# Kernel tuning notes

Hardware: AMD Instinct MI355X
Metric: run time of the kernel (lower is better)

Reference implementation:

```python
import jax, jax.numpy as jnp
import numpy as np

H = 256   # hidden_size
IN = 2    # adding-problem input features
B, T = 128, 1024


def setup_inputs() -> dict:
    key = jax.random.key(0)
    ks = jax.random.split(key, 12)
    sc = 1.0 / np.sqrt(H)
    u = lambda k, shape: jax.random.uniform(k, shape, minval=-sc, maxval=sc, dtype=jnp.float32)
    return {
        "x": jax.random.normal(ks[0], (B, T, IN), dtype=jnp.float32),
        # GRU weights (torch layout: [3H, in], gate order r, z, n)
        "W_ih": u(ks[1], (3 * H, IN)),
        "W_hh": u(ks[2], (3 * H, H)),
        "b_ih": u(ks[3], (3 * H,)),
        "b_hh": u(ks[4], (3 * H,)),
        # adaptive momentum coefficient beta_t = sigmoid(x W + h U + b)
        "Wb_x": u(ks[5], (IN, 1)),
        "Wb_h": u(ks[6], (H, 1)),
        "b_beta": jnp.zeros((1,), dtype=jnp.float32),
        # momentum step size s (learnable scalar)
        "s": jnp.ones((), dtype=jnp.float32),
        # read-out head Linear(H, 1)
        "W_head": u(ks[7], (1, H)),
        "b_head": u(ks[8], (1,)),
    }


def reference(x, W_ih, W_hh, b_ih, b_hh, Wb_x, Wb_h, b_beta, s, W_head, b_head):
    Bm = x.shape[0]

    def step(carry, x_t):
        h, v = carry                                    # h: [B,H], v: [B,3H]
        beta = jax.nn.sigmoid(x_t @ Wb_x + h @ Wb_h + b_beta)   # [B,1]
        p = x_t @ W_ih.T + b_ih                         # input projection [B,3H]
        v = beta * v + s * p                            # momentum buffer
        gh = h @ W_hh.T + b_hh                          # hidden projection [B,3H]
        vr, vz, vn = jnp.split(v, 3, axis=-1)
        hr, hz, hn = jnp.split(gh, 3, axis=-1)
        r = jax.nn.sigmoid(vr + hr)
        z = jax.nn.sigmoid(vz + hz)
        n = jnp.tanh(vn + r * hn)
        h_new = (1.0 - z) * n + z * h
        return (h_new, v), beta[:, 0]

    h0 = jnp.zeros((Bm, H), dtype=x.dtype)
    v0 = jnp.zeros((Bm, 3 * H), dtype=x.dtype)
    (hT, _), betas = jax.lax.scan(step, (h0, v0), jnp.transpose(x, (1, 0, 2)))
    out = hT @ W_head.T + b_head                        # head on last timestep, [B,1]
    return (out, betas.T)                               # betas: [B,T]
```

## Files before the change

### kernel.cpp

```cpp
#include <hip/hip_runtime.h>

#define HID 256
#define TLEN 1024
#define BATCH 128

typedef _Float16 half2_t __attribute__((ext_vector_type(2)));

__device__ __forceinline__ float fexp2(float x) { return __builtin_amdgcn_exp2f(x); }
__device__ __forceinline__ float frcp(float x)  { return __builtin_amdgcn_rcpf(x); }
__device__ __forceinline__ float fast_sigmoid(float x) {
  return frcp(1.0f + fexp2(-1.442695040888963f * x));
}
__device__ __forceinline__ float fast_tanh(float x) {
  float e = fexp2(2.885390081777927f * x);
  return 1.0f - 2.0f * frcp(e + 1.0f);
}
__device__ __forceinline__ float dot2acc(half2_t a, half2_t b, float c) {
  return __builtin_amdgcn_fdot2(a, b, c, false);
}

#if defined(__has_builtin) && __has_builtin(__builtin_amdgcn_sdot4)
#define SDOT4(a, b, c) __builtin_amdgcn_sdot4((int)(a), (int)(b), (c), false)
#else
__device__ __forceinline__ int SDOT4(int a, int b, int c) {
#pragma unroll
  for (int e = 0; e < 4; ++e)
    c += ((a << (24 - 8 * e)) >> 24) * ((b << (24 - 8 * e)) >> 24);
  return c;
}
#endif

#define DPP_ADD_F(var, ctrl, rmask)                                            \
  var += __builtin_bit_cast(float, __builtin_amdgcn_update_dpp(                \
      0, __builtin_bit_cast(int, var), (ctrl), (rmask), 0xf, true))
#define DPP_ADD_I(var, ctrl, rmask)                                            \
  var += __builtin_amdgcn_update_dpp(0, (var), (ctrl), (rmask), 0xf, true)

__device__ __forceinline__ float wave_sum63_f(float p) {
  DPP_ADD_F(p, 0x111, 0xf);
  DPP_ADD_F(p, 0x112, 0xf);
  DPP_ADD_F(p, 0x114, 0xf);
  DPP_ADD_F(p, 0x118, 0xf);
  DPP_ADD_F(p, 0x142, 0xa);
  DPP_ADD_F(p, 0x143, 0xc);
  return p;
}
__device__ __forceinline__ int wave_sum63_i(int p) {
  DPP_ADD_I(p, 0x111, 0xf);
  DPP_ADD_I(p, 0x112, 0xf);
  DPP_ADD_I(p, 0x114, 0xf);
  DPP_ADD_I(p, 0x118, 0xf);
  DPP_ADD_I(p, 0x142, 0xa);
  DPP_ADD_I(p, 0x143, 0xc);
  return p;
}

__global__ void quant_whh(const float* __restrict__ W_hh,
                          const float* __restrict__ Wb_h,
                          uint4* __restrict__ wq,
                          float* __restrict__ scales,
                          unsigned* __restrict__ wbq,
                          float* __restrict__ wbscale) {
  const int r = blockIdx.x * 256 + threadIdx.x;
  if (r < 768) {
    const float* row = W_hh + (size_t)r * HID;
    float amax = 0.0f;
    for (int k = 0; k < HID; ++k) amax = fmaxf(amax, fabsf(row[k]));
    amax = fmaxf(amax, 1e-20f);
    scales[r] = amax / 127.0f;
    const float inv = 127.0f / amax;
    const int g = r >> 8, dd = r & 255;
    for (int c = 0; c < 16; ++c) {
      unsigned w[4];
#pragma unroll
      for (int u = 0; u < 4; ++u) {
        unsigned bb = 0;
#pragma unroll
        for (int e = 0; e < 4; ++e) {
          int qv = (int)rintf(row[16 * c + 4 * u + e] * inv);
          bb |= (unsigned)(qv & 0xff) << (8 * e);
        }
        w[u] = bb;
      }
      wq[(size_t)dd * 48 + g * 16 + c] = uint4{w[0], w[1], w[2], w[3]};
    }
  } else if (r < 832) {
    float amax = 0.0f;
    for (int k = 0; k < HID; ++k) amax = fmaxf(amax, fabsf(Wb_h[k]));
    amax = fmaxf(amax, 1e-20f);
    const float inv = 127.0f / amax;
    const int i = r - 768;
    unsigned bb = 0;
#pragma unroll
    for (int e = 0; e < 4; ++e) {
      int qv = (int)rintf(Wb_h[4 * i + e] * inv);
      bb |= (unsigned)(qv & 0xff) << (8 * e);
    }
    wbq[i] = bb;
    if (i == 0) wbscale[0] = (amax / 127.0f) * (1.0f / 127.0f);
  }
}

__global__
__attribute__((amdgpu_flat_work_group_size(256, 256)))
__attribute__((amdgpu_waves_per_eu(1, 1)))
void momgru_persistent(const float* __restrict__ x,
                       const float* __restrict__ W_ih,
                       const float* __restrict__ b_ih,
                       const float* __restrict__ b_hh,
                       const float* __restrict__ Wb_x,
                       const float* __restrict__ b_beta,
                       const float* __restrict__ s_ptr,
                       const float* __restrict__ W_head,
                       const float* __restrict__ b_head,
                       const uint4* __restrict__ wq,
                       const float* __restrict__ scales,
                       const unsigned* __restrict__ wbq,
                       const float* __restrict__ wbscale,
                       float* __restrict__ out)
{
  const int b    = blockIdx.x;
  const int tid  = threadIdx.x;
  const int lane = tid & 63;
  const int wv   = tid >> 6;

  __shared__ unsigned hq[2][64];
  __shared__ float    red[4];

  const uint4* wqt = wq + (size_t)tid * 48;
  uint4 wr[16], wz[16], wn[16];
#pragma unroll
  for (int j = 0; j < 16; ++j) wr[j] = wqt[j];
#pragma unroll
  for (int j = 0; j < 16; ++j) wz[j] = wqt[16 + j];
#pragma unroll
  for (int j = 0; j < 16; ++j) wn[j] = wqt[32 + j];

  const float sv = s_ptr[0];
  const half2_t wih_r = half2_t{(_Float16)(sv * W_ih[2 * tid]),             (_Float16)(sv * W_ih[2 * tid + 1])};
  const half2_t wih_z = half2_t{(_Float16)(sv * W_ih[2 * (HID + tid)]),     (_Float16)(sv * W_ih[2 * (HID + tid) + 1])};
  const half2_t wih_n = half2_t{(_Float16)(sv * W_ih[2 * (2 * HID + tid)]), (_Float16)(sv * W_ih[2 * (2 * HID + tid) + 1])};
  const float bih_r = sv * b_ih[tid], bih_z = sv * b_ih[HID + tid], bih_n = sv * b_ih[2 * HID + tid];
  const float bhh_r = b_hh[tid], bhh_z = b_hh[HID + tid], bhh_n = b_hh[2 * HID + tid];
  const float sc_r = scales[tid] * (1.0f / 127.0f);
  const float sc_z = scales[HID + tid] * (1.0f / 127.0f);
  const float sc_n = scales[2 * HID + tid] * (1.0f / 127.0f);
  const half2_t wbx2 = half2_t{(_Float16)Wb_x[0], (_Float16)Wb_x[1]};
  const float bbeta = b_beta[0];
  const unsigned wbq_l = wbq[lane];
  const float wbsc = wbscale[0];

  if (tid < 128) reinterpret_cast<unsigned*>(hq)[tid] = 0u;
  if (tid < 4) red[tid] = 0.0f;
  float h_old = 0.0f, vr = 0.0f, vz = 0.0f, vn = 0.0f;
  float* betas = out + BATCH;
  const float2* xg2 = reinterpret_cast<const float2*>(x + (size_t)b * TLEN * 2);
  float2 xv = xg2[0];
  __syncthreads();

  int cur = 0;
  for (int t = 0; t < TLEN; ++t) {
    const unsigned hw_l = reinterpret_cast<const unsigned*>(hq[cur])[lane];
    int hwb_i = SDOT4(hw_l, wbq_l, 0);
    hwb_i = wave_sum63_i(hwb_i);

    int ar0 = 0, az0 = 0, an0 = 0, ar1 = 0, az1 = 0, an1 = 0;
    const int4* hb = reinterpret_cast<const int4*>(hq[cur]);
#pragma unroll
    for (int c = 0; c < 8; ++c) {
      const int4 h0 = hb[2 * c];
      const int4 h1 = hb[2 * c + 1];
      ar0 = SDOT4(h0.x, wr[2 * c].x, ar0);
      az0 = SDOT4(h0.x, wz[2 * c].x, az0);
      an0 = SDOT4(h0.x, wn[2 * c].x, an0);
      ar1 = SDOT4(h1.x, wr[2 * c + 1].x, ar1);
      az1 = SDOT4(h1.x, wz[2 * c + 1].x, az1);
      an1 = SDOT4(h1.x, wn[2 * c + 1].x, an1);
      ar0 = SDOT4(h0.y, wr[2 * c].y, ar0);
      az0 = SDOT4(h0.y, wz[2 * c].y, az0);
      an0 = SDOT4(h0.y, wn[2 * c].y, an0);
      ar1 = SDOT4(h1.y, wr[2 * c + 1].y, ar1);
      az1 = SDOT4(h1.y, wz[2 * c + 1].y, az1);
      an1 = SDOT4(h1.y, wn[2 * c + 1].y, an1);
      ar0 = SDOT4(h0.z, wr[2 * c].z, ar0);
      az0 = SDOT4(h0.z, wz[2 * c].z, az0);
      an0 = SDOT4(h0.z, wn[2 * c].z, an0);
      ar1 = SDOT4(h1.z, wr[2 * c + 1].z, ar1);
      az1 = SDOT4(h1.z, wz[2 * c + 1].z, az1);
      an1 = SDOT4(h1.z, wn[2 * c + 1].z, an1);
      ar0 = SDOT4(h0.w, wr[2 * c].w, ar0);
      az0 = SDOT4(h0.w, wz[2 * c].w, az0);
      an0 = SDOT4(h0.w, wn[2 * c].w, an0);
      ar1 = SDOT4(h1.w, wr[2 * c + 1].w, ar1);
      az1 = SDOT4(h1.w, wz[2 * c + 1].w, az1);
      an1 = SDOT4(h1.w, wn[2 * c + 1].w, an1);
    }
    const int ar = ar0 + ar1, az = az0 + az1, an = an0 + an1;

    const float hWb = (float)__builtin_amdgcn_readlane(hwb_i, 63) * wbsc;
    const half2_t x2 = half2_t{(_Float16)xv.x, (_Float16)xv.y};
    xv = xg2[(t + 1 < TLEN) ? t + 1 : t];
    const float beta = fast_sigmoid(dot2acc(x2, wbx2, hWb + bbeta));
    vr = beta * vr + dot2acc(x2, wih_r, bih_r);
    vz = beta * vz + dot2acc(x2, wih_z, bih_z);
    vn = beta * vn + dot2acc(x2, wih_n, bih_n);

    const float r = fast_sigmoid(vr + (float)ar * sc_r + bhh_r);
    const float z = fast_sigmoid(vz + (float)az * sc_z + bhh_z);
    const float n = fast_tanh(vn + r * ((float)an * sc_n + bhh_n));
    h_old = (1.0f - z) * n + z * h_old;

    const int nxt = cur ^ 1;
    const int qb = (int)rintf(h_old * 127.0f);
    reinterpret_cast<unsigned char*>(hq[nxt])[tid] = (unsigned char)(qb & 0xff);

    if (tid == 0) betas[(size_t)b * TLEN + t] = beta;

    __syncthreads();
    cur = nxt;
  }

  float hp = h_old * W_head[tid];
  hp = wave_sum63_f(hp);
  if (lane == 63) red[wv] = hp;
  __syncthreads();
  if (tid == 0) out[b] = red[0] + red[1] + red[2] + red[3] + b_head[0];
}

extern "C" void kernel_launch(void* const* d_in, const int* in_sizes, int n_in,
                              void* d_out, int out_size, void* d_ws, size_t ws_size,
                              hipStream_t stream) {
  const float* x      = (const float*)d_in[0];
  const float* W_ih   = (const float*)d_in[1];
  const float* W_hh   = (const float*)d_in[2];
  const float* b_ih   = (const float*)d_in[3];
  const float* b_hh   = (const float*)d_in[4];
  const float* Wb_x   = (const float*)d_in[5];
  const float* Wb_h   = (const float*)d_in[6];
  const float* b_beta = (const float*)d_in[7];
  const float* s      = (const float*)d_in[8];
  const float* W_head = (const float*)d_in[9];
  const float* b_head = (const float*)d_in[10];
  float* out = (float*)d_out;

  char* wsb = (char*)d_ws;
  uint4*    wq      = (uint4*)wsb;
  float*    scales  = (float*)(wsb + 196608);
  unsigned* wbq     = (unsigned*)(wsb + 199680);
  float*    wbscale = (float*)(wsb + 199936);

  quant_whh<<<dim3(4), dim3(256), 0, stream>>>(W_hh, Wb_h, wq, scales, wbq, wbscale);
  momgru_persistent<<<dim3(BATCH), dim3(256), 0, stream>>>(
      x, W_ih, b_ih, b_hh, Wb_x, b_beta, s, W_head, b_head,
      (const uint4*)wq, (const float*)scales, (const unsigned*)wbq,
      (const float*)wbscale, out);
}
```

Before: 823.0 us.

## Split GRU gates across 768 threads per block with LDS gate exchange

Each block now runs 768 threads, one per gate row (r, z, n), instead of 256 threads each computing all three gates. Per-thread register weights and dot-product work drop threefold, and r/z activations are passed to the n-gate threads through shared memory. The beta projection switches from an int8 SDOT reduction to an fp32 wave reduction over the new h, done by the n-gate waves and carried to the next step. In exchange each timestep now needs two block barriers instead of one, and fewer lanes do useful work in the n-gate phase.

```diff
diff --git a/kernel.cpp b/kernel.cpp
--- a/kernel.cpp
+++ b/kernel.cpp
@@ -33,8 +33,6 @@
 #define DPP_ADD_F(var, ctrl, rmask)                                            \
   var += __builtin_bit_cast(float, __builtin_amdgcn_update_dpp(                \
       0, __builtin_bit_cast(int, var), (ctrl), (rmask), 0xf, true))
-#define DPP_ADD_I(var, ctrl, rmask)                                            \
-  var += __builtin_amdgcn_update_dpp(0, (var), (ctrl), (rmask), 0xf, true)
 
 __device__ __forceinline__ float wave_sum63_f(float p) {
   DPP_ADD_F(p, 0x111, 0xf);
@@ -45,186 +43,149 @@
   DPP_ADD_F(p, 0x143, 0xc);
   return p;
 }
-__device__ __forceinline__ int wave_sum63_i(int p) {
-  DPP_ADD_I(p, 0x111, 0xf);
-  DPP_ADD_I(p, 0x112, 0xf);
-  DPP_ADD_I(p, 0x114, 0xf);
-  DPP_ADD_I(p, 0x118, 0xf);
-  DPP_ADD_I(p, 0x142, 0xa);
-  DPP_ADD_I(p, 0x143, 0xc);
-  return p;
-}
 
 __global__ void quant_whh(const float* __restrict__ W_hh,
-                          const float* __restrict__ Wb_h,
                           uint4* __restrict__ wq,
-                          float* __restrict__ scales,
-                          unsigned* __restrict__ wbq,
-                          float* __restrict__ wbscale) {
+                          float* __restrict__ scales) {
   const int r = blockIdx.x * 256 + threadIdx.x;
-  if (r < 768) {
-    const float* row = W_hh + (size_t)r * HID;
-    float amax = 0.0f;
-    for (int k = 0; k < HID; ++k) amax = fmaxf(amax, fabsf(row[k]));
-    amax = fmaxf(amax, 1e-20f);
-    scales[r] = amax / 127.0f;
-    const float inv = 127.0f / amax;
-    const int g = r >> 8, dd = r & 255;
-    for (int c = 0; c < 16; ++c) {
-      unsigned w[4];
-#pragma unroll
-      for (int u = 0; u < 4; ++u) {
-        unsigned bb = 0;
-#pragma unroll
-        for (int e = 0; e < 4; ++e) {
-          int qv = (int)rintf(row[16 * c + 4 * u + e] * inv);
-          bb |= (unsigned)(qv & 0xff) << (8 * e);
-        }
-        w[u] = bb;
+  const float* row = W_hh + (size_t)r * HID;
+  float amax = 0.0f;
+  for (int k = 0; k < HID; ++k) amax = fmaxf(amax, fabsf(row[k]));
+  amax = fmaxf(amax, 1e-20f);
+  scales[r] = amax / 127.0f;
+  const float inv = 127.0f / amax;
+  for (int c = 0; c < 16; ++c) {
+    unsigned w[4];
+#pragma unroll
+    for (int u = 0; u < 4; ++u) {
+      unsigned bb = 0;
+#pragma unroll
+      for (int e = 0; e < 4; ++e) {
+        int qv = (int)rintf(row[16 * c + 4 * u + e] * inv);
+        bb |= (unsigned)(qv & 0xff) << (8 * e);
       }
-      wq[(size_t)dd * 48 + g * 16 + c] = uint4{w[0], w[1], w[2], w[3]};
+      w[u] = bb;
     }
-  } else if (r < 832) {
-    float amax = 0.0f;
-    for (int k = 0; k < HID; ++k) amax = fmaxf(amax, fabsf(Wb_h[k]));
-    amax = fmaxf(amax, 1e-20f);
-    const float inv = 127.0f / amax;
-    const int i = r - 768;
-    unsigned bb = 0;
-#pragma unroll
-    for (int e = 0; e < 4; ++e) {
-      int qv = (int)rintf(Wb_h[4 * i + e] * inv);
-      bb |= (unsigned)(qv & 0xff) << (8 * e);
-    }
-    wbq[i] = bb;
-    if (i == 0) wbscale[0] = (amax / 127.0f) * (1.0f / 127.0f);
+    wq[(size_t)r * 16 + c] = uint4{w[0], w[1], w[2], w[3]};
   }
 }
 
 __global__
-__attribute__((amdgpu_flat_work_group_size(256, 256)))
-__attribute__((amdgpu_waves_per_eu(1, 1)))
+__attribute__((amdgpu_flat_work_group_size(768, 768)))
 void momgru_persistent(const float* __restrict__ x,
                        const float* __restrict__ W_ih,
                        const float* __restrict__ b_ih,
                        const float* __restrict__ b_hh,
                        const float* __restrict__ Wb_x,
+                       const float* __restrict__ Wb_h,
                        const float* __restrict__ b_beta,
                        const float* __restrict__ s_ptr,
                        const float* __restrict__ W_head,
                        const float* __restrict__ b_head,
                        const uint4* __restrict__ wq,
                        const float* __restrict__ scales,
-                       const unsigned* __restrict__ wbq,
-                       const float* __restrict__ wbscale,
                        float* __restrict__ out)
 {
   const int b    = blockIdx.x;
   const int tid  = threadIdx.x;
   const int lane = tid & 63;
   const int wv   = tid >> 6;
-
-  __shared__ unsigned hq[2][64];
-  __shared__ float    red[4];
-
-  const uint4* wqt = wq + (size_t)tid * 48;
-  uint4 wr[16], wz[16], wn[16];
-#pragma unroll
-  for (int j = 0; j < 16; ++j) wr[j] = wqt[j];
-#pragma unroll
-  for (int j = 0; j < 16; ++j) wz[j] = wqt[16 + j];
-#pragma unroll
-  for (int j = 0; j < 16; ++j) wn[j] = wqt[32 + j];
+  const int g    = tid >> 8;
+  const int d    = tid & 255;
+
+  __shared__ __align__(16) unsigned hq[64];
+  __shared__ float  rz[2][256];
+  __shared__ float4 red4;
+  __shared__ float  headred[4];
+
+  const uint4* wqt = wq + (size_t)tid * 16;
+  uint4 w[16];
+#pragma unroll
+  for (int j = 0; j < 16; ++j) w[j] = wqt[j];
 
   const float sv = s_ptr[0];
-  const half2_t wih_r = half2_t{(_Float16)(sv * W_ih[2 * tid]),             (_Float16)(sv * W_ih[2 * tid + 1])};
-  const half2_t wih_z = half2_t{(_Float16)(sv * W_ih[2 * (HID + tid)]),     (_Float16)(sv * W_ih[2 * (HID + tid) + 1])};
-  const half2_t wih_n = half2_t{(_Float16)(sv * W_ih[2 * (2 * HID + tid)]), (_Float16)(sv * W_ih[2 * (2 * HID + tid) + 1])};
-  const float bih_r = sv * b_ih[tid], bih_z = sv * b_ih[HID + tid], bih_n = sv * b_ih[2 * HID + tid];
-  const float bhh_r = b_hh[tid], bhh_z = b_hh[HID + tid], bhh_n = b_hh[2 * HID + tid];
-  const float sc_r = scales[tid] * (1.0f / 127.0f);
-  const float sc_z = scales[HID + tid] * (1.0f / 127.0f);
-  const float sc_n = scales[2 * HID + tid] * (1.0f / 127.0f);
+  const half2_t wih2 = half2_t{(_Float16)(sv * W_ih[2 * tid]),
+                               (_Float16)(sv * W_ih[2 * tid + 1])};
+  const float bih = sv * b_ih[tid];
+  const float bhh = b_hh[tid];
+  const float sc  = scales[tid] * (1.0f / 127.0f);
   const half2_t wbx2 = half2_t{(_Float16)Wb_x[0], (_Float16)Wb_x[1]};
   const float bbeta = b_beta[0];
-  const unsigned wbq_l = wbq[lane];
-  const float wbsc = wbscale[0];
-
-  if (tid < 128) reinterpret_cast<unsigned*>(hq)[tid] = 0u;
-  if (tid < 4) red[tid] = 0.0f;
-  float h_old = 0.0f, vr = 0.0f, vz = 0.0f, vn = 0.0f;
+  const float wbh   = Wb_h[d];
+
+  if (tid < 64) hq[tid] = 0u;
+  if (tid == 0) red4 = make_float4(bbeta, 0.0f, 0.0f, 0.0f);
+  float v = 0.0f, h_old = 0.0f;
   float* betas = out + BATCH;
   const float2* xg2 = reinterpret_cast<const float2*>(x + (size_t)b * TLEN * 2);
   float2 xv = xg2[0];
   __syncthreads();
 
-  int cur = 0;
   for (int t = 0; t < TLEN; ++t) {
-    const unsigned hw_l = reinterpret_cast<const unsigned*>(hq[cur])[lane];
-    int hwb_i = SDOT4(hw_l, wbq_l, 0);
-    hwb_i = wave_sum63_i(hwb_i);
-
-    int ar0 = 0, az0 = 0, an0 = 0, ar1 = 0, az1 = 0, an1 = 0;
-    const int4* hb = reinterpret_cast<const int4*>(hq[cur]);
-#pragma unroll
-    for (int c = 0; c < 8; ++c) {
-      const int4 h0 = hb[2 * c];
-      const int4 h1 = hb[2 * c + 1];
-      ar0 = SDOT4(h0.x, wr[2 * c].x, ar0);
-      az0 = SDOT4(h0.x, wz[2 * c].x, az0);
-      an0 = SDOT4(h0.x, wn[2 * c].x, an0);
-      ar1 = SDOT4(h1.x, wr[2 * c + 1].x, ar1);
-      az1 = SDOT4(h1.x, wz[2 * c + 1].x, az1);
-      an1 = SDOT4(h1.x, wn[2 * c + 1].x, an1);
-      ar0 = SDOT4(h0.y, wr[2 * c].y, ar0);
-      az0 = SDOT4(h0.y, wz[2 * c].y, az0);
-      an0 = SDOT4(h0.y, wn[2 * c].y, an0);
-      ar1 = SDOT4(h1.y, wr[2 * c + 1].y, ar1);
-      az1 = SDOT4(h1.y, wz[2 * c + 1].y, az1);
-      an1 = SDOT4(h1.y, wn[2 * c + 1].y, an1);
-      ar0 = SDOT4(h0.z, wr[2 * c].z, ar0);
-      az0 = SDOT4(h0.z, wz[2 * c].z, az0);
-      an0 = SDOT4(h0.z, wn[2 * c].z, an0);
-      ar1 = SDOT4(h1.z, wr[2 * c + 1].z, ar1);
-      az1 = SDOT4(h1.z, wz[2 * c + 1].z, az1);
-      an1 = SDOT4(h1.z, wn[2 * c + 1].z, an1);
-      ar0 = SDOT4(h0.w, wr[2 * c].w, ar0);
-      az0 = SDOT4(h0.w, wz[2 * c].w, az0);
-      an0 = SDOT4(h0.w, wn[2 * c].w, an0);
-      ar1 = SDOT4(h1.w, wr[2 * c + 1].w, ar1);
-      az1 = SDOT4(h1.w, wz[2 * c + 1].w, az1);
-      an1 = SDOT4(h1.w, wn[2 * c + 1].w, an1);
-    }
-    const int ar = ar0 + ar1, az = az0 + az1, an = an0 + an1;
-
-    const float hWb = (float)__builtin_amdgcn_readlane(hwb_i, 63) * wbsc;
+    const float4 rr = red4;
+    const float hwb = (rr.x + rr.y) + (rr.z + rr.w);
     const half2_t x2 = half2_t{(_Float16)xv.x, (_Float16)xv.y};
     xv = xg2[(t + 1 < TLEN) ? t + 1 : t];
-    const float beta = fast_sigmoid(dot2acc(x2, wbx2, hWb + bbeta));
-    vr = beta * vr + dot2acc(x2, wih_r, bih_r);
-    vz = beta * vz + dot2acc(x2, wih_z, bih_z);
-    vn = beta * vn + dot2acc(x2, wih_n, bih_n);
-
-    const float r = fast_sigmoid(vr + (float)ar * sc_r + bhh_r);
-    const float z = fast_sigmoid(vz + (float)az * sc_z + bhh_z);
-    const float n = fast_tanh(vn + r * ((float)an * sc_n + bhh_n));
-    h_old = (1.0f - z) * n + z * h_old;
-
-    const int nxt = cur ^ 1;
-    const int qb = (int)rintf(h_old * 127.0f);
-    reinterpret_cast<unsigned char*>(hq[nxt])[tid] = (unsigned char)(qb & 0xff);
-
+    const float beta = fast_sigmoid(dot2acc(x2, wbx2, hwb));
+    v = beta * v + dot2acc(x2, wih2, bih);
     if (tid == 0) betas[(size_t)b * TLEN + t] = beta;
 
+    const int4* hb = reinterpret_cast<const int4*>(hq);
+    int a0 = 0, a1 = 0, a2 = 0, a3 = 0;
+#pragma unroll
+    for (int c = 0; c < 4; ++c) {
+      const int4 h0 = hb[4 * c + 0];
+      const int4 h1 = hb[4 * c + 1];
+      const int4 h2 = hb[4 * c + 2];
+      const int4 h3 = hb[4 * c + 3];
+      a0 = SDOT4(h0.x, w[4 * c + 0].x, a0);
+      a1 = SDOT4(h1.x, w[4 * c + 1].x, a1);
+      a2 = SDOT4(h2.x, w[4 * c + 2].x, a2);
+      a3 = SDOT4(h3.x, w[4 * c + 3].x, a3);
+      a0 = SDOT4(h0.y, w[4 * c + 0].y, a0);
+      a1 = SDOT4(h1.y, w[4 * c + 1].y, a1);
+      a2 = SDOT4(h2.y, w[4 * c + 2].y, a2);
+      a3 = SDOT4(h3.y, w[4 * c + 3].y, a3);
+      a0 = SDOT4(h0.z, w[4 * c + 0].z, a0);
+      a1 = SDOT4(h1.z, w[4 * c + 1].z, a1);
+      a2 = SDOT4(h2.z, w[4 * c + 2].z, a2);
+      a3 = SDOT4(h3.z, w[4 * c + 3].z, a3);
+      a0 = SDOT4(h0.w, w[4 * c + 0].w, a0);
+      a1 = SDOT4(h1.w, w[4 * c + 1].w, a1);
+      a2 = SDOT4(h2.w, w[4 * c + 2].w, a2);
+      a3 = SDOT4(h3.w, w[4 * c + 3].w, a3);
+    }
+    const int a = (a0 + a1) + (a2 + a3);
+    const float ga = fmaf((float)a, sc, bhh);
+
+    if (g < 2) rz[g][d] = fast_sigmoid(v + ga);
     __syncthreads();
-    cur = nxt;
+
+    if (g == 2) {
+      const float r_ = rz[0][d];
+      const float z_ = rz[1][d];
+      const float n_ = fast_tanh(fmaf(r_, ga, v));
+      h_old = fmaf(z_, h_old - n_, n_);
+      const int q = (int)rintf(h_old * 127.0f);
+      reinterpret_cast<unsigned char*>(hq)[d] = (unsigned char)(q & 0xff);
+      float p = h_old * wbh;
+      p = wave_sum63_f(p);
+      if (lane == 63) {
+        const float pv = (wv == 8) ? p + bbeta : p;
+        reinterpret_cast<float*>(&red4)[wv - 8] = pv;
+      }
+    }
+    __syncthreads();
   }
 
-  float hp = h_old * W_head[tid];
-  hp = wave_sum63_f(hp);
-  if (lane == 63) red[wv] = hp;
+  if (g == 2) {
+    float hp = h_old * W_head[d];
+    hp = wave_sum63_f(hp);
+    if (lane == 63) headred[wv - 8] = hp;
+  }
   __syncthreads();
-  if (tid == 0) out[b] = red[0] + red[1] + red[2] + red[3] + b_head[0];
+  if (tid == 0)
+    out[b] = ((headred[0] + headred[1]) + (headred[2] + headred[3])) + b_head[0];
 }
 
 extern "C" void kernel_launch(void* const* d_in, const int* in_sizes, int n_in,
@@ -244,14 +205,11 @@
   float* out = (float*)d_out;
 
   char* wsb = (char*)d_ws;
-  uint4*    wq      = (uint4*)wsb;
-  float*    scales  = (float*)(wsb + 196608);
-  unsigned* wbq     = (unsigned*)(wsb + 199680);
-  float*    wbscale = (float*)(wsb + 199936);
-
-  quant_whh<<<dim3(4), dim3(256), 0, stream>>>(W_hh, Wb_h, wq, scales, wbq, wbscale);
-  momgru_persistent<<<dim3(BATCH), dim3(256), 0, stream>>>(
-      x, W_ih, b_ih, b_hh, Wb_x, b_beta, s, W_head, b_head,
-      (const uint4*)wq, (const float*)scales, (const unsigned*)wbq,
-      (const float*)wbscale, out);
-}
+  uint4* wq     = (uint4*)wsb;
+  float* scales = (float*)(wsb + 196608);
+
+  quant_whh<<<dim3(3), dim3(256), 0, stream>>>(W_hh, wq, scales);
+  momgru_persistent<<<dim3(BATCH), dim3(768), 0, stream>>>(
+      x, W_ih, b_ih, b_hh, Wb_x, Wb_h, b_beta, s, W_head, b_head,
+      (const uint4*)wq, (const float*)scales, out);
+}
```

After: 997.4 us. 1.21x slower.

## Split hidden-dim K reduction across two thread halves with shared partial sums

Applied to the files above, without the earlier changes.

The per-block thread count doubles to 512, and each hidden unit's dot product over the 256-wide hidden state is split between two threads that each handle half of K. The second half writes partial sums to shared memory and the first half combines them and applies the gate nonlinearities. The weight layout is changed to row-major to match. This halves the serial SDOT4 chain per thread and the register footprint per thread, at the cost of an extra __syncthreads and a shared-memory round trip every timestep.

```diff
diff --git a/kernel.cpp b/kernel.cpp
--- a/kernel.cpp
+++ b/kernel.cpp
@@ -69,7 +69,6 @@
     amax = fmaxf(amax, 1e-20f);
     scales[r] = amax / 127.0f;
     const float inv = 127.0f / amax;
-    const int g = r >> 8, dd = r & 255;
     for (int c = 0; c < 16; ++c) {
       unsigned w[4];
 #pragma unroll
@@ -82,7 +81,7 @@
         }
         w[u] = bb;
       }
-      wq[(size_t)dd * 48 + g * 16 + c] = uint4{w[0], w[1], w[2], w[3]};
+      wq[(size_t)r * 16 + c] = uint4{w[0], w[1], w[2], w[3]};
     }
   } else if (r < 832) {
     float amax = 0.0f;
@@ -102,8 +101,8 @@
 }
 
 __global__
-__attribute__((amdgpu_flat_work_group_size(256, 256)))
-__attribute__((amdgpu_waves_per_eu(1, 1)))
+__attribute__((amdgpu_flat_work_group_size(512, 512)))
+__attribute__((amdgpu_waves_per_eu(2, 2)))
 void momgru_persistent(const float* __restrict__ x,
                        const float* __restrict__ W_ih,
                        const float* __restrict__ b_ih,
@@ -121,30 +120,35 @@
 {
   const int b    = blockIdx.x;
   const int tid  = threadIdx.x;
+  const int sub  = tid >> 8;
+  const int d    = tid & 255;
   const int lane = tid & 63;
   const int wv   = tid >> 6;
 
-  __shared__ unsigned hq[2][64];
-  __shared__ float    red[4];
-
-  const uint4* wqt = wq + (size_t)tid * 48;
-  uint4 wr[16], wz[16], wn[16];
-#pragma unroll
-  for (int j = 0; j < 16; ++j) wr[j] = wqt[j];
-#pragma unroll
-  for (int j = 0; j < 16; ++j) wz[j] = wqt[16 + j];
-#pragma unroll
-  for (int j = 0; j < 16; ++j) wn[j] = wqt[32 + j];
+  __shared__ __align__(16) unsigned hq[2][64];
+  __shared__ int   parts[3 * HID];
+  __shared__ float red[4];
+
+  const uint4* wr_p = wq + ((size_t)(0 * HID + d) * 16 + sub * 8);
+  const uint4* wz_p = wq + ((size_t)(1 * HID + d) * 16 + sub * 8);
+  const uint4* wn_p = wq + ((size_t)(2 * HID + d) * 16 + sub * 8);
+  uint4 wr[8], wz[8], wn[8];
+#pragma unroll
+  for (int j = 0; j < 8; ++j) wr[j] = wr_p[j];
+#pragma unroll
+  for (int j = 0; j < 8; ++j) wz[j] = wz_p[j];
+#pragma unroll
+  for (int j = 0; j < 8; ++j) wn[j] = wn_p[j];
 
   const float sv = s_ptr[0];
-  const half2_t wih_r = half2_t{(_Float16)(sv * W_ih[2 * tid]),             (_Float16)(sv * W_ih[2 * tid + 1])};
-  const half2_t wih_z = half2_t{(_Float16)(sv * W_ih[2 * (HID + tid)]),     (_Float16)(sv * W_ih[2 * (HID + tid) + 1])};
-  const half2_t wih_n = half2_t{(_Float16)(sv * W_ih[2 * (2 * HID + tid)]), (_Float16)(sv * W_ih[2 * (2 * HID + tid) + 1])};
-  const float bih_r = sv * b_ih[tid], bih_z = sv * b_ih[HID + tid], bih_n = sv * b_ih[2 * HID + tid];
-  const float bhh_r = b_hh[tid], bhh_z = b_hh[HID + tid], bhh_n = b_hh[2 * HID + tid];
-  const float sc_r = scales[tid] * (1.0f / 127.0f);
-  const float sc_z = scales[HID + tid] * (1.0f / 127.0f);
-  const float sc_n = scales[2 * HID + tid] * (1.0f / 127.0f);
+  const half2_t wih_r = half2_t{(_Float16)(sv * W_ih[2 * d]),             (_Float16)(sv * W_ih[2 * d + 1])};
+  const half2_t wih_z = half2_t{(_Float16)(sv * W_ih[2 * (HID + d)]),     (_Float16)(sv * W_ih[2 * (HID + d) + 1])};
+  const half2_t wih_n = half2_t{(_Float16)(sv * W_ih[2 * (2 * HID + d)]), (_Float16)(sv * W_ih[2 * (2 * HID + d) + 1])};
+  const float bih_r = sv * b_ih[d], bih_z = sv * b_ih[HID + d], bih_n = sv * b_ih[2 * HID + d];
+  const float bhh_r = b_hh[d], bhh_z = b_hh[HID + d], bhh_n = b_hh[2 * HID + d];
+  const float sc_r = scales[d] * (1.0f / 127.0f);
+  const float sc_z = scales[HID + d] * (1.0f / 127.0f);
+  const float sc_n = scales[2 * HID + d] * (1.0f / 127.0f);
   const half2_t wbx2 = half2_t{(_Float16)Wb_x[0], (_Float16)Wb_x[1]};
   const float bbeta = b_beta[0];
   const unsigned wbq_l = wbq[lane];
@@ -155,19 +159,23 @@
   float h_old = 0.0f, vr = 0.0f, vz = 0.0f, vn = 0.0f;
   float* betas = out + BATCH;
   const float2* xg2 = reinterpret_cast<const float2*>(x + (size_t)b * TLEN * 2);
-  float2 xv = xg2[0];
+  float2 xv;
+  if (sub == 0) xv = xg2[0];
   __syncthreads();
 
   int cur = 0;
   for (int t = 0; t < TLEN; ++t) {
-    const unsigned hw_l = reinterpret_cast<const unsigned*>(hq[cur])[lane];
-    int hwb_i = SDOT4(hw_l, wbq_l, 0);
-    hwb_i = wave_sum63_i(hwb_i);
-
+    int hwb_i = 0;
+    if (sub == 0) {
+      const unsigned hw_l = reinterpret_cast<const unsigned*>(hq[cur])[lane];
+      hwb_i = SDOT4(hw_l, wbq_l, 0);
+      hwb_i = wave_sum63_i(hwb_i);
+    }
+
+    const int4* hb = reinterpret_cast<const int4*>(hq[cur]) + sub * 8;
     int ar0 = 0, az0 = 0, an0 = 0, ar1 = 0, az1 = 0, an1 = 0;
-    const int4* hb = reinterpret_cast<const int4*>(hq[cur]);
-#pragma unroll
-    for (int c = 0; c < 8; ++c) {
+#pragma unroll
+    for (int c = 0; c < 4; ++c) {
       const int4 h0 = hb[2 * c];
       const int4 h1 = hb[2 * c + 1];
       ar0 = SDOT4(h0.x, wr[2 * c].x, ar0);
@@ -197,34 +205,43 @@
     }
     const int ar = ar0 + ar1, az = az0 + az1, an = an0 + an1;
 
-    const float hWb = (float)__builtin_amdgcn_readlane(hwb_i, 63) * wbsc;
-    const half2_t x2 = half2_t{(_Float16)xv.x, (_Float16)xv.y};
-    xv = xg2[(t + 1 < TLEN) ? t + 1 : t];
-    const float beta = fast_sigmoid(dot2acc(x2, wbx2, hWb + bbeta));
-    vr = beta * vr + dot2acc(x2, wih_r, bih_r);
-    vz = beta * vz + dot2acc(x2, wih_z, bih_z);
-    vn = beta * vn + dot2acc(x2, wih_n, bih_n);
-
-    const float r = fast_sigmoid(vr + (float)ar * sc_r + bhh_r);
-    const float z = fast_sigmoid(vz + (float)az * sc_z + bhh_z);
-    const float n = fast_tanh(vn + r * ((float)an * sc_n + bhh_n));
-    h_old = (1.0f - z) * n + z * h_old;
-
-    const int nxt = cur ^ 1;
-    const int qb = (int)rintf(h_old * 127.0f);
-    reinterpret_cast<unsigned char*>(hq[nxt])[tid] = (unsigned char)(qb & 0xff);
-
-    if (tid == 0) betas[(size_t)b * TLEN + t] = beta;
-
+    float beta = 0.0f;
+    if (sub == 1) {
+      parts[d] = ar;
+      parts[HID + d] = az;
+      parts[2 * HID + d] = an;
+    } else {
+      const float hWb = (float)__builtin_amdgcn_readlane(hwb_i, 63) * wbsc;
+      const half2_t x2 = half2_t{(_Float16)xv.x, (_Float16)xv.y};
+      xv = xg2[(t + 1 < TLEN) ? t + 1 : t];
+      beta = fast_sigmoid(dot2acc(x2, wbx2, hWb + bbeta));
+      vr = beta * vr + dot2acc(x2, wih_r, bih_r);
+      vz = beta * vz + dot2acc(x2, wih_z, bih_z);
+      vn = beta * vn + dot2acc(x2, wih_n, bih_n);
+    }
     __syncthreads();
-    cur = nxt;
+
+    if (sub == 0) {
+      const float r = fast_sigmoid(vr + (float)(ar + parts[d]) * sc_r + bhh_r);
+      const float z = fast_sigmoid(vz + (float)(az + parts[HID + d]) * sc_z + bhh_z);
+      const float n = fast_tanh(vn + r * ((float)(an + parts[2 * HID + d]) * sc_n + bhh_n));
+      h_old = (1.0f - z) * n + z * h_old;
+      const int qb = (int)rintf(h_old * 127.0f);
+      reinterpret_cast<unsigned char*>(hq[cur ^ 1])[d] = (unsigned char)(qb & 0xff);
+      if (tid == 0) betas[(size_t)b * TLEN + t] = beta;
+    }
+    __syncthreads();
+    cur ^= 1;
   }
 
-  float hp = h_old * W_head[tid];
-  hp = wave_sum63_f(hp);
-  if (lane == 63) red[wv] = hp;
+  if (sub == 0) {
+    float hp = h_old * W_head[d];
+    hp = wave_sum63_f(hp);
+    if (lane == 63) red[wv] = hp;
+  }
   __syncthreads();
-  if (tid == 0) out[b] = red[0] + red[1] + red[2] + red[3] + b_head[0];
+  if (tid == 0)
+    out[b] = ((red[0] + red[1]) + (red[2] + red[3])) + b_head[0];
 }
 
 extern "C" void kernel_launch(void* const* d_in, const int* in_sizes, int n_in,
@@ -250,7 +267,7 @@
   float*    wbscale = (float*)(wsb + 199936);
 
   quant_whh<<<dim3(4), dim3(256), 0, stream>>>(W_hh, Wb_h, wq, scales, wbq, wbscale);
-  momgru_persistent<<<dim3(BATCH), dim3(256), 0, stream>>>(
+  momgru_persistent<<<dim3(BATCH), dim3(512), 0, stream>>>(
       x, W_ih, b_ih, b_hh, Wb_x, b_beta, s, W_head, b_head,
       (const uint4*)wq, (const float*)scales, (const unsigned*)wbq,
       (const float*)wbscale, out);
```

After: 889.5 us. 8.1% more time.

## Compute int8 recurrent matvec with MFMA 16x16x64 instead of per-thread SDOT4

Applied to the files above, without the earlier changes.

The hidden-to-hidden int8 matvec moves from per-thread sdot4 chains to MFMA i8 16x16x64 instructions. Each wave holds its 64 rows per gate as B-fragments, and the A fragment replicates the quantized h vector across rows. The quantized weight layout changes to row-major so the fragments load directly. Accumulator row 0 goes through a shared gm buffer and is redistributed to the owning threads. This aims to cut the VALU-bound dot-product cost per timestep, but 15 of the 16 MFMA output rows are wasted work and an extra LDS round trip is added.

```diff
diff --git a/kernel.cpp b/kernel.cpp
--- a/kernel.cpp
+++ b/kernel.cpp
@@ -5,6 +5,7 @@
 #define BATCH 128
 
 typedef _Float16 half2_t __attribute__((ext_vector_type(2)));
+typedef int i32x4 __attribute__((ext_vector_type(4)));
 
 __device__ __forceinline__ float fexp2(float x) { return __builtin_amdgcn_exp2f(x); }
 __device__ __forceinline__ float frcp(float x)  { return __builtin_amdgcn_rcpf(x); }
@@ -69,7 +70,6 @@
     amax = fmaxf(amax, 1e-20f);
     scales[r] = amax / 127.0f;
     const float inv = 127.0f / amax;
-    const int g = r >> 8, dd = r & 255;
     for (int c = 0; c < 16; ++c) {
       unsigned w[4];
 #pragma unroll
@@ -82,7 +82,7 @@
         }
         w[u] = bb;
       }
-      wq[(size_t)dd * 48 + g * 16 + c] = uint4{w[0], w[1], w[2], w[3]};
+      wq[(size_t)r * 16 + c] = uint4{w[0], w[1], w[2], w[3]};
     }
   } else if (r < 832) {
     float amax = 0.0f;
@@ -123,18 +123,22 @@
   const int tid  = threadIdx.x;
   const int lane = tid & 63;
   const int wv   = tid >> 6;
-
-  __shared__ unsigned hq[2][64];
-  __shared__ float    red[4];
-
-  const uint4* wqt = wq + (size_t)tid * 48;
-  uint4 wr[16], wz[16], wn[16];
-#pragma unroll
-  for (int j = 0; j < 16; ++j) wr[j] = wqt[j];
-#pragma unroll
-  for (int j = 0; j < 16; ++j) wz[j] = wqt[16 + j];
-#pragma unroll
-  for (int j = 0; j < 16; ++j) wn[j] = wqt[32 + j];
+  const int l15  = lane & 15;
+  const int lg   = lane >> 4;
+
+  __shared__ __align__(16) unsigned hq[2][64];
+  __shared__ int   gm[3 * HID];
+  __shared__ float red[4];
+
+  i32x4 bw[12][4];
+#pragma unroll
+  for (int t = 0; t < 12; ++t) {
+    const int gate = t >> 2, i = t & 3;
+    const int row = gate * 256 + 64 * wv + 16 * i + l15;
+#pragma unroll
+    for (int c = 0; c < 4; ++c)
+      bw[t][c] = *reinterpret_cast<const i32x4*>(&wq[(size_t)row * 16 + 4 * c + lg]);
+  }
 
   const float sv = s_ptr[0];
   const half2_t wih_r = half2_t{(_Float16)(sv * W_ih[2 * tid]),             (_Float16)(sv * W_ih[2 * tid + 1])};
@@ -160,42 +164,31 @@
 
   int cur = 0;
   for (int t = 0; t < TLEN; ++t) {
+    const char* hqb = reinterpret_cast<const char*>(hq[cur]);
+    const i32x4 af0 = *reinterpret_cast<const i32x4*>(hqb + 0   + 16 * lg);
+    const i32x4 af1 = *reinterpret_cast<const i32x4*>(hqb + 64  + 16 * lg);
+    const i32x4 af2 = *reinterpret_cast<const i32x4*>(hqb + 128 + 16 * lg);
+    const i32x4 af3 = *reinterpret_cast<const i32x4*>(hqb + 192 + 16 * lg);
+
     const unsigned hw_l = reinterpret_cast<const unsigned*>(hq[cur])[lane];
     int hwb_i = SDOT4(hw_l, wbq_l, 0);
     hwb_i = wave_sum63_i(hwb_i);
 
-    int ar0 = 0, az0 = 0, an0 = 0, ar1 = 0, az1 = 0, an1 = 0;
-    const int4* hb = reinterpret_cast<const int4*>(hq[cur]);
-#pragma unroll
-    for (int c = 0; c < 8; ++c) {
-      const int4 h0 = hb[2 * c];
-      const int4 h1 = hb[2 * c + 1];
-      ar0 = SDOT4(h0.x, wr[2 * c].x, ar0);
-      az0 = SDOT4(h0.x, wz[2 * c].x, az0);
-      an0 = SDOT4(h0.x, wn[2 * c].x, an0);
-      ar1 = SDOT4(h1.x, wr[2 * c + 1].x, ar1);
-      az1 = SDOT4(h1.x, wz[2 * c + 1].x, az1);
-      an1 = SDOT4(h1.x, wn[2 * c + 1].x, an1);
-      ar0 = SDOT4(h0.y, wr[2 * c].y, ar0);
-      az0 = SDOT4(h0.y, wz[2 * c].y, az0);
-      an0 = SDOT4(h0.y, wn[2 * c].y, an0);
-      ar1 = SDOT4(h1.y, wr[2 * c + 1].y, ar1);
-      az1 = SDOT4(h1.y, wz[2 * c + 1].y, az1);
-      an1 = SDOT4(h1.y, wn[2 * c + 1].y, an1);
-      ar0 = SDOT4(h0.z, wr[2 * c].z, ar0);
-      az0 = SDOT4(h0.z, wz[2 * c].z, az0);
-      an0 = SDOT4(h0.z, wn[2 * c].z, an0);
-      ar1 = SDOT4(h1.z, wr[2 * c + 1].z, ar1);
-      az1 = SDOT4(h1.z, wz[2 * c + 1].z, az1);
-      an1 = SDOT4(h1.z, wn[2 * c + 1].z, an1);
-      ar0 = SDOT4(h0.w, wr[2 * c].w, ar0);
-      az0 = SDOT4(h0.w, wz[2 * c].w, az0);
-      an0 = SDOT4(h0.w, wn[2 * c].w, an0);
-      ar1 = SDOT4(h1.w, wr[2 * c + 1].w, ar1);
-      az1 = SDOT4(h1.w, wz[2 * c + 1].w, az1);
-      an1 = SDOT4(h1.w, wn[2 * c + 1].w, an1);
-    }
-    const int ar = ar0 + ar1, az = az0 + az1, an = an0 + an1;
+    i32x4 acc[12];
+#pragma unroll
+    for (int tt = 0; tt < 12; ++tt) acc[tt] = i32x4{0, 0, 0, 0};
+#pragma unroll
+    for (int tt = 0; tt < 12; ++tt)
+      acc[tt] = __builtin_amdgcn_mfma_i32_16x16x64_i8(af0, bw[tt][0], acc[tt], 0, 0, 0);
+#pragma unroll
+    for (int tt = 0; tt < 12; ++tt)
+      acc[tt] = __builtin_amdgcn_mfma_i32_16x16x64_i8(af1, bw[tt][1], acc[tt], 0, 0, 0);
+#pragma unroll
+    for (int tt = 0; tt < 12; ++tt)
+      acc[tt] = __builtin_amdgcn_mfma_i32_16x16x64_i8(af2, bw[tt][2], acc[tt], 0, 0, 0);
+#pragma unroll
+    for (int tt = 0; tt < 12; ++tt)
+      acc[tt] = __builtin_amdgcn_mfma_i32_16x16x64_i8(af3, bw[tt][3], acc[tt], 0, 0, 0);
 
     const float hWb = (float)__builtin_amdgcn_readlane(hwb_i, 63) * wbsc;
     const half2_t x2 = half2_t{(_Float16)xv.x, (_Float16)xv.y};
@@ -205,6 +198,17 @@
     vz = beta * vz + dot2acc(x2, wih_z, bih_z);
     vn = beta * vn + dot2acc(x2, wih_n, bih_n);
 
+    if (lane < 16) {
+#pragma unroll
+      for (int tt = 0; tt < 12; ++tt) {
+        const int gate = tt >> 2, i = tt & 3;
+        gm[gate * 256 + 64 * wv + 16 * i + l15] = acc[tt][0];
+      }
+    }
+    const int ar = gm[tid];
+    const int az = gm[HID + tid];
+    const int an = gm[2 * HID + tid];
+
     const float r = fast_sigmoid(vr + (float)ar * sc_r + bhh_r);
     const float z = fast_sigmoid(vz + (float)az * sc_z + bhh_z);
     const float n = fast_tanh(vn + r * ((float)an * sc_n + bhh_n));
@@ -224,7 +228,8 @@
   hp = wave_sum63_f(hp);
   if (lane == 63) red[wv] = hp;
   __syncthreads();
-  if (tid == 0) out[b] = red[0] + red[1] + red[2] + red[3] + b_head[0];
+  if (tid == 0)
+    out[b] = ((red[0] + red[1]) + (red[2] + red[3])) + b_head[0];
 }
 
 extern "C" void kernel_launch(void* const* d_in, const int* in_sizes, int n_in,
```

Result: slower. 928.1 us (+12.8%).
